# Optimization experiments

Measured on AMD Instinct MI355X. Metric: run time of the kernel, lower is better.

## Reference

```python
import jax, jax.numpy as jnp
import numpy as np

B, C, H, W = 2, 256, 48, 48
HIDDEN, NUM_HEADS = 512, 8
HEAD_DIM = HIDDEN // NUM_HEADS
EPS = 1e-5


def setup_inputs() -> dict:
    key = jax.random.key(0)
    ks = jax.random.split(key, 16)
    inp = {
        'modal1_feat': jax.random.normal(ks[0], (B, C, H, W), jnp.float32),
        'modal2_feat': jax.random.normal(ks[1], (B, C, H, W), jnp.float32),
    }
    s = 0.02  # weight init scale
    names = ['wq1', 'wk1', 'wv1', 'wq2', 'wk2', 'wv2']
    for i, nm in enumerate(names):
        inp[nm] = jax.random.normal(ks[2 + i], (HIDDEN, C), jnp.float32) * s
        inp['b' + nm[1:]] = jnp.zeros((HIDDEN,), jnp.float32)
    inp['wo1'] = jax.random.normal(ks[8], (C, HIDDEN), jnp.float32) * s
    inp['bo1'] = jnp.zeros((C,), jnp.float32)
    inp['wo2'] = jax.random.normal(ks[9], (C, HIDDEN), jnp.float32) * s
    inp['bo2'] = jnp.zeros((C,), jnp.float32)
    inp['ln1_g'] = jnp.ones((C,), jnp.float32)
    inp['ln1_b'] = jnp.zeros((C,), jnp.float32)
    inp['ln2_g'] = jnp.ones((C,), jnp.float32)
    inp['ln2_b'] = jnp.zeros((C,), jnp.float32)
    inp['wf'] = jax.random.normal(ks[10], (C, 2 * C), jnp.float32) * s
    inp['bf'] = jnp.zeros((C,), jnp.float32)
    inp['bn_g'] = jnp.ones((C,), jnp.float32)
    inp['bn_b'] = jnp.zeros((C,), jnp.float32)
    inp['bn_mean'] = jnp.zeros((C,), jnp.float32)
    inp['bn_var'] = jnp.ones((C,), jnp.float32)
    return inp


def _conv1x1(x, w, b):
    return jnp.einsum('bchw,oc->bohw', x, w) + b[None, :, None, None]


def _ln_channels(x, g, b):
    # LayerNorm over channel dim (x: [B,C,H,W]) applied in NHWC layout
    xc = x.transpose(0, 2, 3, 1)
    mu = xc.mean(-1, keepdims=True)
    var = ((xc - mu) ** 2).mean(-1, keepdims=True)
    y = (xc - mu) / jnp.sqrt(var + EPS) * g + b
    return y.transpose(0, 3, 1, 2)


def reference(modal1_feat, modal2_feat, wq1, bq1, wk1, bk1, wv1, bv1,
              wq2, bq2, wk2, bk2, wv2, bv2, wo1, bo1, wo2, bo2,
              ln1_g, ln1_b, ln2_g, ln2_b, wf, bf, bn_g, bn_b, bn_mean, bn_var):
    b_, c1, h1, w1 = modal1_feat.shape
    hw = h1 * w1
    scale = HEAD_DIM ** -0.5

    def as_q(t):  # [B,hidden,H,W] -> [B,h,L,d]
        return t.reshape(b_, NUM_HEADS, HEAD_DIM, hw).transpose(0, 1, 3, 2)

    def as_k(t):  # [B,h,d,L]
        return t.reshape(b_, NUM_HEADS, HEAD_DIM, hw)

    q1 = as_q(_conv1x1(modal1_feat, wq1, bq1))
    k1 = as_k(_conv1x1(modal1_feat, wk1, bk1))
    v1 = as_q(_conv1x1(modal1_feat, wv1, bv1))
    q2 = as_q(_conv1x1(modal2_feat, wq2, bq2))
    k2 = as_k(_conv1x1(modal2_feat, wk2, bk2))
    v2 = as_q(_conv1x1(modal2_feat, wv2, bv2))

    a12 = jax.nn.softmax(jnp.einsum('bhld,bhdm->bhlm', q1, k2) * scale, axis=-1)
    o1 = jnp.einsum('bhlm,bhmd->bhld', a12, v2).transpose(0, 1, 3, 2).reshape(b_, HIDDEN, h1, w1)
    a21 = jax.nn.softmax(jnp.einsum('bhld,bhdm->bhlm', q2, k1) * scale, axis=-1)
    o2 = jnp.einsum('bhlm,bhmd->bhld', a21, v1).transpose(0, 1, 3, 2).reshape(b_, HIDDEN, h1, w1)

    mod1_cross = _conv1x1(o1, wo1, bo1)
    mod2_cross = _conv1x1(o2, wo2, bo2)

    m1 = _ln_channels(modal1_feat + mod1_cross, ln1_g, ln1_b)
    m2 = _ln_channels(modal2_feat + mod2_cross, ln2_g, ln2_b)

    fused = jnp.concatenate([m1, m2], axis=1)
    f = _conv1x1(fused, wf, bf)
    # BatchNorm2d in eval mode (running stats)
    f = (f - bn_mean[None, :, None, None]) / jnp.sqrt(bn_var + EPS)[None, :, None, None]
    f = f * bn_g[None, :, None, None] + bn_b[None, :, None, None]
    return jax.nn.relu(f)
```

## Files before the change

### kernel.cpp

```cpp
#include <hip/hip_runtime.h>
#include <hip/hip_bf16.h>

#define HW_N 2304
#define EPS_F 1e-5f
#define QSCALE 0.18033688011112043f

typedef float f32x4 __attribute__((ext_vector_type(4)));
typedef short short8v __attribute__((ext_vector_type(8)));
typedef __bf16 bf16x8 __attribute__((ext_vector_type(8)));
typedef unsigned short u16;

__device__ __forceinline__ f32x4 mfma_bf16(bf16x8 a, bf16x8 b, f32x4 c) {
    return __builtin_amdgcn_mfma_f32_16x16x32_bf16(a, b, c, 0, 0, 0);
}
__device__ __forceinline__ bf16x8 ld8(const void* p) {
    return __builtin_bit_cast(bf16x8, *(const short8v*)p);
}
__device__ __forceinline__ unsigned short bfbits(float v) {
    return __builtin_bit_cast(unsigned short, __float2bfloat16(v));
}
__device__ __forceinline__ float b2f(u16 u) {
    unsigned x = (unsigned)u << 16;
    return __builtin_bit_cast(float, x);
}
__device__ __forceinline__ unsigned pack2(float lo, float hi) {
    return (unsigned)bfbits(lo) | ((unsigned)bfbits(hi) << 16);
}
__device__ __forceinline__ float max4(f32x4 v) {
    return fmaxf(fmaxf(v.x, v.y), fmaxf(v.z, v.w));
}
__device__ __forceinline__ float sum4(f32x4 v) {
    return (v.x + v.y) + (v.z + v.w);
}

struct WPtrs { const float* s[9]; u16* d[9]; };

__global__ __launch_bounds__(256)
void conv_w_kernel(WPtrs p)
{
    const int j = blockIdx.z;
    const float* s = p.s[j];
    u16* d = p.d[j];
    const int i = (blockIdx.x * 256 + threadIdx.x) * 4;
    const float4 v = *(const float4*)(s + i);
    ushort4 pk;
    pk.x = bfbits(v.x); pk.y = bfbits(v.y); pk.z = bfbits(v.z); pk.w = bfbits(v.w);
    *(ushort4*)(d + i) = pk;
}

__global__ __launch_bounds__(256)
void prep_modal_kernel(const float* __restrict__ m1, const float* __restrict__ m2,
                       u16* __restrict__ t1, u16* __restrict__ t2)
{
    const int l0 = blockIdx.x * 64, c0 = blockIdx.y * 64;
    const int which = blockIdx.z >> 1, b = blockIdx.z & 1;
    const float* src = (which ? m2 : m1) + ((long long)b * 256 + c0) * HW_N + l0;
    u16* dst = (which ? t2 : t1) + ((long long)b * HW_N + l0) * 256 + c0;

    __shared__ float tile[64][65];
    const int t = threadIdx.x;
    const int r = t >> 4, cq = (t & 15) * 4;
#pragma unroll
    for (int i = 0; i < 4; ++i) {
        const int row = r + i * 16;
        const float4 v = *(const float4*)(src + (long long)row * HW_N + cq);
        tile[row][cq + 0] = v.x; tile[row][cq + 1] = v.y;
        tile[row][cq + 2] = v.z; tile[row][cq + 3] = v.w;
    }
    __syncthreads();
#pragma unroll
    for (int i = 0; i < 4; ++i) {
        const int lr = r + i * 16;
        ushort4 pk;
        pk.x = bfbits(tile[cq + 0][lr]);
        pk.y = bfbits(tile[cq + 1][lr]);
        pk.z = bfbits(tile[cq + 2][lr]);
        pk.w = bfbits(tile[cq + 3][lr]);
        *(ushort4*)(dst + (long long)lr * 256 + cq) = pk;
    }
}

struct GArgs {
    const u16* W[6];
    const float* bias[6];
    const u16* X[2];
    const u16* R[2];
    u16* outQ[2]; u16* outK[2]; u16* outV[2];
    float* outT[2];
    float* outC;
    const float *bnm, *bnv, *bng, *bnb;
};

template<int MODE>
__global__ __launch_bounds__(256)
void gemm_mfma(GArgs g)
{
    constexpr int KD = (MODE == 0) ? 256 : 512;
    constexpr int NS = KD / 32;
    const int z = blockIdx.y;
    const int j = blockIdx.z;
    const int mt_b = blockIdx.x / 18;
    const int nt_b = blockIdx.x - mt_b * 18;
    const int m0 = mt_b * 128, n0 = nt_b * 128;

    const u16* Wb = g.W[(MODE == 2) ? 0 : j];
    const u16* Xb0 = (MODE == 0) ? g.X[(j < 3) ? 0 : 1]
                                 : ((MODE == 1) ? g.X[j] : nullptr);

    __shared__ u16 Als[4096];
    __shared__ u16 Bls[4096];

    const int tid = threadIdx.x;
    const int w = tid >> 6, lane = tid & 63;
    const int l16 = lane & 15, lg = lane >> 4;

    const int ar0 = (((tid >> 6) << 4) | (tid & 15));
    const int k8 = (tid >> 4) & 3;

    short8v sa0, sa1, sb0, sb1;

    auto stage = [&](int kb) {
        const int koff = kb + k8 * 8;
        sa0 = *(const short8v*)(Wb + (long long)(m0 + ar0) * KD + koff);
        sa1 = *(const short8v*)(Wb + (long long)(m0 + ar0 + 64) * KD + koff);
        if constexpr (MODE == 0) {
            const u16* p = Xb0 + ((long long)z * HW_N + n0 + ar0) * 256 + koff;
            sb0 = *(const short8v*)p;
            sb1 = *(const short8v*)(p + 64LL * 256);
        } else if constexpr (MODE == 1) {
            const int head = kb >> 6;
            const u16* p = Xb0 + (((long long)z * 8 + head) * HW_N + n0 + ar0) * 64 + (koff & 63);
            sb0 = *(const short8v*)p;
            sb1 = *(const short8v*)(p + 64LL * 64);
        } else {
            const u16* Xb = (kb < 256) ? g.X[0] : g.X[1];
            const u16* p = Xb + ((long long)z * HW_N + n0 + ar0) * 256 + (koff & 255);
            sb0 = *(const short8v*)p;
            sb1 = *(const short8v*)(p + 64LL * 256);
        }
    };

    f32x4 acc[4][4];
#pragma unroll
    for (int a = 0; a < 4; ++a)
#pragma unroll
        for (int b = 0; b < 4; ++b) acc[a][b] = f32x4{0.f, 0.f, 0.f, 0.f};

    stage(0);
    for (int s = 0; s < NS; ++s) {
        __syncthreads();
        *(short8v*)((char*)Als + tid * 16) = sa0;
        *(short8v*)((char*)Als + tid * 16 + 4096) = sa1;
        *(short8v*)((char*)Bls + tid * 16) = sb0;
        *(short8v*)((char*)Bls + tid * 16 + 4096) = sb1;
        __syncthreads();
        if (s + 1 < NS) stage((s + 1) * 32);

        bf16x8 bfr[4];
#pragma unroll
        for (int nt = 0; nt < 4; ++nt)
            bfr[nt] = ld8((char*)Bls + ((w & 1) * 4 + nt) * 1024 + lane * 16);
#pragma unroll
        for (int mt = 0; mt < 4; ++mt) {
            const bf16x8 af = ld8((char*)Als + ((w >> 1) * 4 + mt) * 1024 + lane * 16);
#pragma unroll
            for (int nt = 0; nt < 4; ++nt)
                acc[mt][nt] = mfma_bf16(af, bfr[nt], acc[mt][nt]);
        }
    }

    const int mbase = m0 + (w >> 1) * 64 + 4 * lg;
    const int nbase = n0 + (w & 1) * 64 + l16;

    if constexpr (MODE == 0) {
        const int kind = j % 3, which = j / 3;
        const float* Bp = g.bias[j];
        if (kind < 2) {
            u16* T = (kind == 0) ? g.outQ[which] : g.outK[which];
            const float s = (kind == 0) ? QSCALE : 1.0f;
#pragma unroll
            for (int mt = 0; mt < 4; ++mt) {
                const int m = mbase + mt * 16;
                const float4 bv = *(const float4*)(Bp + m);
#pragma unroll
                for (int nt = 0; nt < 4; ++nt) {
                    const int l = nbase + nt * 16;
                    const f32x4 a = acc[mt][nt];
                    ushort4 pk;
                    pk.x = bfbits((a.x + bv.x) * s);
                    pk.y = bfbits((a.y + bv.y) * s);
                    pk.z = bfbits((a.z + bv.z) * s);
                    pk.w = bfbits((a.w + bv.w) * s);
                    *(ushort4*)(T + ((long long)(z * 8 + (m >> 6)) * HW_N + l) * 64 + (m & 63)) = pk;
                }
            }
        } else {
            u16* V = g.outV[which];
#pragma unroll
            for (int mt = 0; mt < 4; ++mt) {
                const int m = mbase + mt * 16;
                const float4 bv = *(const float4*)(Bp + m);
#pragma unroll
                for (int nt = 0; nt < 4; ++nt) {
                    const int l = nbase + nt * 16;
                    const f32x4 a = acc[mt][nt];
                    V[((long long)z * 512 + m + 0) * HW_N + l] = bfbits(a.x + bv.x);
                    V[((long long)z * 512 + m + 1) * HW_N + l] = bfbits(a.y + bv.y);
                    V[((long long)z * 512 + m + 2) * HW_N + l] = bfbits(a.z + bv.z);
                    V[((long long)z * 512 + m + 3) * HW_N + l] = bfbits(a.w + bv.w);
                }
            }
        }
    } else if constexpr (MODE == 1) {
        const float* Bp = g.bias[j];
        const u16* Rb = g.R[j];
        float* Ob = g.outT[j];
#pragma unroll
        for (int mt = 0; mt < 4; ++mt) {
            const int m = mbase + mt * 16;
            const float4 bv = *(const float4*)(Bp + m);
#pragma unroll
            for (int nt = 0; nt < 4; ++nt) {
                const int l = nbase + nt * 16;
                const long long rowoff = ((long long)z * HW_N + l) * 256 + m;
                const ushort4 rv = *(const ushort4*)(Rb + rowoff);
                const f32x4 a = acc[mt][nt];
                float4 o;
                o.x = a.x + bv.x + b2f(rv.x);
                o.y = a.y + bv.y + b2f(rv.y);
                o.z = a.z + bv.z + b2f(rv.z);
                o.w = a.w + bv.w + b2f(rv.w);
                *(float4*)(Ob + rowoff) = o;
            }
        }
    } else {
        const float* Bp = g.bias[0];
#pragma unroll
        for (int mt = 0; mt < 4; ++mt) {
            const int m = mbase + mt * 16;
            const float4 bv = *(const float4*)(Bp + m);
            const float4 mu = *(const float4*)(g.bnm + m);
            const float4 vr = *(const float4*)(g.bnv + m);
            const float4 ga = *(const float4*)(g.bng + m);
            const float4 be = *(const float4*)(g.bnb + m);
            const float sc0 = ga.x * rsqrtf(vr.x + EPS_F), sh0 = be.x - mu.x * sc0;
            const float sc1 = ga.y * rsqrtf(vr.y + EPS_F), sh1 = be.y - mu.y * sc1;
            const float sc2 = ga.z * rsqrtf(vr.z + EPS_F), sh2 = be.z - mu.z * sc2;
            const float sc3 = ga.w * rsqrtf(vr.w + EPS_F), sh3 = be.w - mu.w * sc3;
#pragma unroll
            for (int nt = 0; nt < 4; ++nt) {
                const int l = nbase + nt * 16;
                const f32x4 a = acc[mt][nt];
                float* O = g.outC + (long long)z * 256 * HW_N + l;
                O[(long long)(m + 0) * HW_N] = fmaxf((a.x + bv.x) * sc0 + sh0, 0.f);
                O[(long long)(m + 1) * HW_N] = fmaxf((a.y + bv.y) * sc1 + sh1, 0.f);
                O[(long long)(m + 2) * HW_N] = fmaxf((a.z + bv.z) * sc2 + sh2, 0.f);
                O[(long long)(m + 3) * HW_N] = fmaxf((a.w + bv.w) * sc3 + sh3, 0.f);
            }
        }
    }
}

__global__ __launch_bounds__(256)
void attn_mfma_kernel(const u16* __restrict__ qt0, const u16* __restrict__ kt0,
                      const u16* __restrict__ v0b,
                      const u16* __restrict__ qt1, const u16* __restrict__ kt1,
                      const u16* __restrict__ v1b,
                      u16* __restrict__ oat0T, u16* __restrict__ oat1T)
{
    const int flat = blockIdx.x;
    const int virt = (flat & 7) * 144 + (flat >> 3);
    const int lt = virt % 36;
    const int h = (virt / 36) & 7;
    const int zz = virt / 288;
    const int b = zz >> 1, dir = zz & 1;

    const u16* QT = dir ? qt1 : qt0;
    const u16* KT = dir ? kt0 : kt1;
    const u16* V  = dir ? v0b : v1b;

    const long long bh = (long long)(b * 8 + h);
    const u16* Qb = QT + bh * HW_N * 64;
    const u16* Kb = KT + bh * HW_N * 64;
    const u16* Vb = V + ((long long)b * 512 + h * 64) * HW_N;

    const int tid = threadIdx.x;
    const int w = tid >> 6, lane = tid & 63;
    const int l16 = lane & 15, lg = lane >> 4;
    const int l0 = lt * 64;

    __shared__ u16 Ks[64 * 64];
    __shared__ u16 Vs[64 * 64];
    __shared__ u16 Ps[4][16 * 72];

    bf16x8 qf0, qf1;
    {
        const u16* qrow = Qb + (long long)(l0 + 16 * w + l16) * 64 + 8 * lg;
        qf0 = ld8(qrow);
        qf1 = ld8(qrow + 32);
    }

    f32x4 acc0 = {0.f, 0.f, 0.f, 0.f}, acc1 = acc0, acc2 = acc0, acc3 = acc0;
    float m_run = -1e30f, s_run = 0.f;

    const int rsub = lane >> 3;
    const int csub = (lane & 7) * 8;
    const int r0 = 16 * w + rsub, r1 = r0 + 8;
    const int swz0 = (csub * 2) ^ ((r0 & 7) << 4);
    const int swz1 = (csub * 2) ^ ((r1 & 7) << 4);
    const int cb0 = (16 * lg) ^ ((l16 & 7) << 4);
    const int cb1 = (16 * lg + 64) ^ ((l16 & 7) << 4);

    short8v ka, kb2, va, vb2;
    {
        const u16* kbase = Kb + (long long)(16 * w) * 64;
        ka  = *(const short8v*)(kbase + (long long)rsub * 64 + csub);
        kb2 = *(const short8v*)(kbase + (long long)(8 + rsub) * 64 + csub);
        const u16* vbase = Vb + (long long)(16 * w + rsub) * HW_N + csub;
        va  = *(const short8v*)(vbase);
        vb2 = *(const short8v*)(vbase + 8LL * HW_N);
    }

    char* prow = (char*)&Ps[w][0] + 144 * l16;

    for (int t = 0; t < 36; ++t) {
        if (t) __syncthreads();
        *(short8v*)((char*)Ks + r0 * 128 + swz0) = ka;
        *(short8v*)((char*)Ks + r1 * 128 + swz1) = kb2;
        *(short8v*)((char*)Vs + r0 * 128 + swz0) = va;
        *(short8v*)((char*)Vs + r1 * 128 + swz1) = vb2;
        __syncthreads();
        if (t + 1 < 36) {
            const int m0 = (t + 1) * 64;
            const u16* kbase = Kb + (long long)(m0 + 16 * w) * 64;
            ka  = *(const short8v*)(kbase + (long long)rsub * 64 + csub);
            kb2 = *(const short8v*)(kbase + (long long)(8 + rsub) * 64 + csub);
            const u16* vbase = Vb + (long long)(16 * w + rsub) * HW_N + m0 + csub;
            va  = *(const short8v*)(vbase);
            vb2 = *(const short8v*)(vbase + 8LL * HW_N);
        }

        const char* kb_ = (const char*)Ks + l16 * 128;
        f32x4 st0 = {0.f,0.f,0.f,0.f}, st1 = st0, st2 = st0, st3 = st0;
        st0 = mfma_bf16(ld8(kb_ + 0 * 2048 + cb0), qf0, st0);
        st0 = mfma_bf16(ld8(kb_ + 0 * 2048 + cb1), qf1, st0);
        st1 = mfma_bf16(ld8(kb_ + 1 * 2048 + cb0), qf0, st1);
        st1 = mfma_bf16(ld8(kb_ + 1 * 2048 + cb1), qf1, st1);
        st2 = mfma_bf16(ld8(kb_ + 2 * 2048 + cb0), qf0, st2);
        st2 = mfma_bf16(ld8(kb_ + 2 * 2048 + cb1), qf1, st2);
        st3 = mfma_bf16(ld8(kb_ + 3 * 2048 + cb0), qf0, st3);
        st3 = mfma_bf16(ld8(kb_ + 3 * 2048 + cb1), qf1, st3);

        float mx = fmaxf(fmaxf(max4(st0), max4(st1)), fmaxf(max4(st2), max4(st3)));
        mx = fmaxf(mx, __shfl_xor(mx, 16, 64));
        mx = fmaxf(mx, __shfl_xor(mx, 32, 64));
        const float m_new = fmaxf(m_run, mx);
        const float alpha = exp2f(m_run - m_new);

        f32x4 p0, p1, p2, p3;
        p0.x = exp2f(st0.x - m_new); p0.y = exp2f(st0.y - m_new);
        p0.z = exp2f(st0.z - m_new); p0.w = exp2f(st0.w - m_new);
        p1.x = exp2f(st1.x - m_new); p1.y = exp2f(st1.y - m_new);
        p1.z = exp2f(st1.z - m_new); p1.w = exp2f(st1.w - m_new);
        p2.x = exp2f(st2.x - m_new); p2.y = exp2f(st2.y - m_new);
        p2.z = exp2f(st2.z - m_new); p2.w = exp2f(st2.w - m_new);
        p3.x = exp2f(st3.x - m_new); p3.y = exp2f(st3.y - m_new);
        p3.z = exp2f(st3.z - m_new); p3.w = exp2f(st3.w - m_new);

        float psum = sum4(p0) + sum4(p1) + sum4(p2) + sum4(p3);
        psum += __shfl_xor(psum, 16, 64);
        psum += __shfl_xor(psum, 32, 64);
        s_run = s_run * alpha + psum;
        m_run = m_new;
        acc0 *= alpha; acc1 *= alpha; acc2 *= alpha; acc3 *= alpha;

        *(unsigned*)(prow + 8 * lg + 0)   = pack2(p0.x, p0.y);
        *(unsigned*)(prow + 8 * lg + 4)   = pack2(p0.z, p0.w);
        *(unsigned*)(prow + 8 * lg + 32)  = pack2(p1.x, p1.y);
        *(unsigned*)(prow + 8 * lg + 36)  = pack2(p1.z, p1.w);
        *(unsigned*)(prow + 8 * lg + 64)  = pack2(p2.x, p2.y);
        *(unsigned*)(prow + 8 * lg + 68)  = pack2(p2.z, p2.w);
        *(unsigned*)(prow + 8 * lg + 96)  = pack2(p3.x, p3.y);
        *(unsigned*)(prow + 8 * lg + 100) = pack2(p3.z, p3.w);

        bf16x8 pf0 = ld8(prow + 16 * lg);
        bf16x8 pf1 = ld8(prow + 64 + 16 * lg);
        const char* vb_ = (const char*)Vs + l16 * 128;
        acc0 = mfma_bf16(ld8(vb_ + 0 * 2048 + cb0), pf0, acc0);
        acc0 = mfma_bf16(ld8(vb_ + 0 * 2048 + cb1), pf1, acc0);
        acc1 = mfma_bf16(ld8(vb_ + 1 * 2048 + cb0), pf0, acc1);
        acc1 = mfma_bf16(ld8(vb_ + 1 * 2048 + cb1), pf1, acc1);
        acc2 = mfma_bf16(ld8(vb_ + 2 * 2048 + cb0), pf0, acc2);
        acc2 = mfma_bf16(ld8(vb_ + 2 * 2048 + cb1), pf1, acc2);
        acc3 = mfma_bf16(ld8(vb_ + 3 * 2048 + cb0), pf0, acc3);
        acc3 = mfma_bf16(ld8(vb_ + 3 * 2048 + cb1), pf1, acc3);
    }

    const float inv = 1.0f / s_run;
    u16* obase = (dir ? oat1T : oat0T) +
                 ((long long)(b * 8 + h) * HW_N + l0 + 16 * w + l16) * 64;
#define OSTORE(T4, A) { \
    ushort4 pk; \
    pk.x = bfbits(A.x * inv); pk.y = bfbits(A.y * inv); \
    pk.z = bfbits(A.z * inv); pk.w = bfbits(A.w * inv); \
    *(ushort4*)(obase + (T4) * 16 + 4 * lg) = pk; }
    OSTORE(0, acc0) OSTORE(1, acc1) OSTORE(2, acc2) OSTORE(3, acc3)
#undef OSTORE
}

__global__ __launch_bounds__(256)
void ln_t_kernel(const float* __restrict__ mpre0T, const float* __restrict__ mpre1T,
                 const float* __restrict__ g1, const float* __restrict__ b1,
                 const float* __restrict__ g2, const float* __restrict__ b2,
                 u16* __restrict__ mln0T, u16* __restrict__ mln1T)
{
    const int l = blockIdx.x * 64 + (threadIdx.x >> 2);
    const int z = blockIdx.y, dir = blockIdx.z;
    const float* src = (dir ? mpre1T : mpre0T) + ((long long)z * HW_N + l) * 256;
    const float* gg = dir ? g2 : g1;
    const float* bb = dir ? b2 : b1;
    u16* dst = (dir ? mln1T : mln0T) + ((long long)z * HW_N + l) * 256;
    const int q = (threadIdx.x & 3) * 64;

    float4 vbuf[16];
    float sum = 0.f, sq = 0.f;
#pragma unroll
    for (int i = 0; i < 16; ++i) {
        const float4 v = *(const float4*)(src + q + i * 4);
        vbuf[i] = v;
        sum += (v.x + v.y) + (v.z + v.w);
        sq += (v.x * v.x + v.y * v.y) + (v.z * v.z + v.w * v.w);
    }
    sum += __shfl_xor(sum, 1, 64); sum += __shfl_xor(sum, 2, 64);
    sq  += __shfl_xor(sq, 1, 64);  sq  += __shfl_xor(sq, 2, 64);
    const float mean = sum * (1.f / 256.f);
    const float var = sq * (1.f / 256.f) - mean * mean;
    const float rstd = rsqrtf(var + EPS_F);
#pragma unroll
    for (int i = 0; i < 16; ++i) {
        const int c = q + i * 4;
        const float4 gv = *(const float4*)(gg + c);
        const float4 bv = *(const float4*)(bb + c);
        ushort4 pk;
        pk.x = bfbits((vbuf[i].x - mean) * rstd * gv.x + bv.x);
        pk.y = bfbits((vbuf[i].y - mean) * rstd * gv.y + bv.y);
        pk.z = bfbits((vbuf[i].z - mean) * rstd * gv.z + bv.z);
        pk.w = bfbits((vbuf[i].w - mean) * rstd * gv.w + bv.w);
        *(ushort4*)(dst + c) = pk;
    }
}

extern "C" void kernel_launch(void* const* d_in, const int* in_sizes, int n_in,
                              void* d_out, int out_size, void* d_ws, size_t ws_size,
                              hipStream_t stream)
{
    (void)in_sizes; (void)n_in; (void)out_size; (void)ws_size;

    const float* modal1 = (const float*)d_in[0];
    const float* modal2 = (const float*)d_in[1];
    const float* wqkv[6]; const float* bqkv[6];
    for (int j = 0; j < 6; ++j) {
        wqkv[j] = (const float*)d_in[2 + 2 * j];
        bqkv[j] = (const float*)d_in[3 + 2 * j];
    }
    const float* wo1 = (const float*)d_in[14];
    const float* bo1 = (const float*)d_in[15];
    const float* wo2 = (const float*)d_in[16];
    const float* bo2 = (const float*)d_in[17];
    const float* ln1_g = (const float*)d_in[18];
    const float* ln1_b = (const float*)d_in[19];
    const float* ln2_g = (const float*)d_in[20];
    const float* ln2_b = (const float*)d_in[21];
    const float* wf = (const float*)d_in[22];
    const float* bf = (const float*)d_in[23];
    const float* bn_g = (const float*)d_in[24];
    const float* bn_b = (const float*)d_in[25];
    const float* bn_mean = (const float*)d_in[26];
    const float* bn_var = (const float*)d_in[27];

    char* ws = (char*)d_ws;
    size_t off = 0;
    auto alloc = [&](size_t bytes) { char* p = ws + off; off += (bytes + 255) & ~(size_t)255; return p; };

    u16* modalT[2]; u16* wbf[9]; u16* qT[2]; u16* kT[2]; u16* vC[2];
    u16* oatT[2]; float* mpreT[2]; u16* mlnT[2];
    for (int i = 0; i < 2; ++i) modalT[i] = (u16*)alloc(2LL * HW_N * 256 * 2);
    for (int i = 0; i < 9; ++i) wbf[i] = (u16*)alloc(131072 * 2);
    for (int i = 0; i < 2; ++i) qT[i] = (u16*)alloc(2LL * 512 * HW_N * 2);
    for (int i = 0; i < 2; ++i) kT[i] = (u16*)alloc(2LL * 512 * HW_N * 2);
    for (int i = 0; i < 2; ++i) vC[i] = (u16*)alloc(2LL * 512 * HW_N * 2);
    for (int i = 0; i < 2; ++i) oatT[i] = (u16*)alloc(2LL * 512 * HW_N * 2);
    for (int i = 0; i < 2; ++i) mpreT[i] = (float*)alloc(2LL * HW_N * 256 * 4);
    for (int i = 0; i < 2; ++i) mlnT[i] = (u16*)alloc(2LL * HW_N * 256 * 2);

    WPtrs wp;
    for (int j = 0; j < 6; ++j) { wp.s[j] = wqkv[j]; wp.d[j] = wbf[j]; }
    wp.s[6] = wo1; wp.d[6] = wbf[6];
    wp.s[7] = wo2; wp.d[7] = wbf[7];
    wp.s[8] = wf;  wp.d[8] = wbf[8];
    conv_w_kernel<<<dim3(128, 1, 9), 256, 0, stream>>>(wp);
    prep_modal_kernel<<<dim3(36, 4, 4), 256, 0, stream>>>(modal1, modal2, modalT[0], modalT[1]);

    GArgs g0 = {};
    for (int j = 0; j < 6; ++j) { g0.W[j] = wbf[j]; g0.bias[j] = bqkv[j]; }
    g0.X[0] = modalT[0]; g0.X[1] = modalT[1];
    for (int i = 0; i < 2; ++i) { g0.outQ[i] = qT[i]; g0.outK[i] = kT[i]; g0.outV[i] = vC[i]; }
    gemm_mfma<0><<<dim3(72, 2, 6), 256, 0, stream>>>(g0);

    attn_mfma_kernel<<<dim3(36 * 8 * 4), 256, 0, stream>>>(
        qT[0], kT[0], vC[0], qT[1], kT[1], vC[1], oatT[0], oatT[1]);

    GArgs g1a = {};
    g1a.W[0] = wbf[6]; g1a.W[1] = wbf[7];
    g1a.bias[0] = bo1; g1a.bias[1] = bo2;
    g1a.X[0] = oatT[0]; g1a.X[1] = oatT[1];
    g1a.R[0] = modalT[0]; g1a.R[1] = modalT[1];
    g1a.outT[0] = mpreT[0]; g1a.outT[1] = mpreT[1];
    gemm_mfma<1><<<dim3(36, 2, 2), 256, 0, stream>>>(g1a);

    ln_t_kernel<<<dim3(36, 2, 2), 256, 0, stream>>>(
        mpreT[0], mpreT[1], ln1_g, ln1_b, ln2_g, ln2_b, mlnT[0], mlnT[1]);

    GArgs g2a = {};
    g2a.W[0] = wbf[8]; g2a.bias[0] = bf;
    g2a.X[0] = mlnT[0]; g2a.X[1] = mlnT[1];
    g2a.outC = (float*)d_out;
    g2a.bnm = bn_mean; g2a.bnv = bn_var; g2a.bng = bn_g; g2a.bnb = bn_b;
    gemm_mfma<2><<<dim3(36, 2, 1), 256, 0, stream>>>(g2a);
}
```

Measured before the change: 195.0 us.

## Double-buffer K/V tiles in attention, lazy rescale, MFMA row sums, swizzled P

The flash-attention loop now uses double-buffered shared K/V tiles with a two-stage register prefetch, leaving one barrier per iteration instead of two. The online softmax skips the rescale unless the new max exceeds the running max by more than a threshold. Row sums are computed by an extra MFMA against a ones vector instead of shuffle reductions. The P scratch gets an XOR swizzle to cut bank conflicts, and s_setprio is placed around the MFMA blocks. The cost is twice the shared memory for K/V, two extra MFMAs per tile, and softmax sums accumulated from the bf16-rounded probabilities.

```diff
diff --git a/kernel.cpp b/kernel.cpp
--- a/kernel.cpp
+++ b/kernel.cpp
@@ -28,9 +28,6 @@
 }
 __device__ __forceinline__ float max4(f32x4 v) {
     return fmaxf(fmaxf(v.x, v.y), fmaxf(v.z, v.w));
-}
-__device__ __forceinline__ float sum4(f32x4 v) {
-    return (v.x + v.y) + (v.z + v.w);
 }
 
 struct WPtrs { const float* s[9]; u16* d[9]; };
@@ -289,9 +286,9 @@
     const int l16 = lane & 15, lg = lane >> 4;
     const int l0 = lt * 64;
 
-    __shared__ u16 Ks[64 * 64];
-    __shared__ u16 Vs[64 * 64];
-    __shared__ u16 Ps[4][16 * 72];
+    __shared__ u16 Ks[2][64 * 64];
+    __shared__ u16 Vs[2][64 * 64];
+    __shared__ u16 Ps[4][16 * 64];
 
     bf16x8 qf0, qf1;
     {
@@ -299,9 +296,17 @@
         qf0 = ld8(qrow);
         qf1 = ld8(qrow + 32);
     }
+    bf16x8 onesv;
+    {
+        short8v o;
+#pragma unroll
+        for (int i = 0; i < 8; ++i) o[i] = (short)0x3F80;
+        onesv = __builtin_bit_cast(bf16x8, o);
+    }
 
     f32x4 acc0 = {0.f, 0.f, 0.f, 0.f}, acc1 = acc0, acc2 = acc0, acc3 = acc0;
-    float m_run = -1e30f, s_run = 0.f;
+    f32x4 accs = acc0;
+    float m_run = -1e30f;
 
     const int rsub = lane >> 3;
     const int csub = (lane & 7) * 8;
@@ -312,36 +317,41 @@
     const int cb1 = (16 * lg + 64) ^ ((l16 & 7) << 4);
 
     short8v ka, kb2, va, vb2;
-    {
-        const u16* kbase = Kb + (long long)(16 * w) * 64;
+    auto stage = [&](int t) {
+        const int m0 = t * 64;
+        const u16* kbase = Kb + (long long)(m0 + 16 * w) * 64;
         ka  = *(const short8v*)(kbase + (long long)rsub * 64 + csub);
         kb2 = *(const short8v*)(kbase + (long long)(8 + rsub) * 64 + csub);
-        const u16* vbase = Vb + (long long)(16 * w + rsub) * HW_N + csub;
+        const u16* vbase = Vb + (long long)(16 * w + rsub) * HW_N + m0 + csub;
         va  = *(const short8v*)(vbase);
         vb2 = *(const short8v*)(vbase + 8LL * HW_N);
-    }
-
-    char* prow = (char*)&Ps[w][0] + 144 * l16;
+    };
+    auto commit = [&](int buf) {
+        *(short8v*)((char*)Ks[buf] + r0 * 128 + swz0) = ka;
+        *(short8v*)((char*)Ks[buf] + r1 * 128 + swz1) = kb2;
+        *(short8v*)((char*)Vs[buf] + r0 * 128 + swz0) = va;
+        *(short8v*)((char*)Vs[buf] + r1 * 128 + swz1) = vb2;
+    };
+
+    char* Pw = (char*)&Ps[w][0];
+    const int pxor = l16 & 7;
+    const int pw_hi = lg >> 1;
+    const int pw_lo = 8 * (lg & 1);
+    const int prow = l16 * 128;
+    const int pr0 = prow + ((lg ^ pxor) << 4);
+    const int pr1 = prow + (((4 + lg) ^ pxor) << 4);
+
+    stage(0); commit(0); stage(1);
+    __syncthreads();
 
     for (int t = 0; t < 36; ++t) {
-        if (t) __syncthreads();
-        *(short8v*)((char*)Ks + r0 * 128 + swz0) = ka;
-        *(short8v*)((char*)Ks + r1 * 128 + swz1) = kb2;
-        *(short8v*)((char*)Vs + r0 * 128 + swz0) = va;
-        *(short8v*)((char*)Vs + r1 * 128 + swz1) = vb2;
-        __syncthreads();
-        if (t + 1 < 36) {
-            const int m0 = (t + 1) * 64;
-            const u16* kbase = Kb + (long long)(m0 + 16 * w) * 64;
-            ka  = *(const short8v*)(kbase + (long long)rsub * 64 + csub);
-            kb2 = *(const short8v*)(kbase + (long long)(8 + rsub) * 64 + csub);
-            const u16* vbase = Vb + (long long)(16 * w + rsub) * HW_N + m0 + csub;
-            va  = *(const short8v*)(vbase);
-            vb2 = *(const short8v*)(vbase + 8LL * HW_N);
-        }
-
-        const char* kb_ = (const char*)Ks + l16 * 128;
+        const int cur = t & 1;
+        if (t + 1 < 36) commit(cur ^ 1);
+        if (t + 2 < 36) stage(t + 2);
+
+        const char* kb_ = (const char*)Ks[cur] + l16 * 128;
         f32x4 st0 = {0.f,0.f,0.f,0.f}, st1 = st0, st2 = st0, st3 = st0;
+        __builtin_amdgcn_s_setprio(1);
         st0 = mfma_bf16(ld8(kb_ + 0 * 2048 + cb0), qf0, st0);
         st0 = mfma_bf16(ld8(kb_ + 0 * 2048 + cb1), qf1, st0);
         st1 = mfma_bf16(ld8(kb_ + 1 * 2048 + cb0), qf0, st1);
@@ -350,42 +360,45 @@
         st2 = mfma_bf16(ld8(kb_ + 2 * 2048 + cb1), qf1, st2);
         st3 = mfma_bf16(ld8(kb_ + 3 * 2048 + cb0), qf0, st3);
         st3 = mfma_bf16(ld8(kb_ + 3 * 2048 + cb1), qf1, st3);
+        __builtin_amdgcn_s_setprio(0);
 
         float mx = fmaxf(fmaxf(max4(st0), max4(st1)), fmaxf(max4(st2), max4(st3)));
         mx = fmaxf(mx, __shfl_xor(mx, 16, 64));
         mx = fmaxf(mx, __shfl_xor(mx, 32, 64));
-        const float m_new = fmaxf(m_run, mx);
-        const float alpha = exp2f(m_run - m_new);
+        if (!__all(mx <= m_run + 8.f)) {
+            const float m_new = fmaxf(m_run, mx);
+            const float alpha = exp2f(m_run - m_new);
+            acc0 *= alpha; acc1 *= alpha; acc2 *= alpha; acc3 *= alpha;
+            accs *= alpha;
+            m_run = m_new;
+        }
 
         f32x4 p0, p1, p2, p3;
-        p0.x = exp2f(st0.x - m_new); p0.y = exp2f(st0.y - m_new);
-        p0.z = exp2f(st0.z - m_new); p0.w = exp2f(st0.w - m_new);
-        p1.x = exp2f(st1.x - m_new); p1.y = exp2f(st1.y - m_new);
-        p1.z = exp2f(st1.z - m_new); p1.w = exp2f(st1.w - m_new);
-        p2.x = exp2f(st2.x - m_new); p2.y = exp2f(st2.y - m_new);
-        p2.z = exp2f(st2.z - m_new); p2.w = exp2f(st2.w - m_new);
-        p3.x = exp2f(st3.x - m_new); p3.y = exp2f(st3.y - m_new);
-        p3.z = exp2f(st3.z - m_new); p3.w = exp2f(st3.w - m_new);
-
-        float psum = sum4(p0) + sum4(p1) + sum4(p2) + sum4(p3);
-        psum += __shfl_xor(psum, 16, 64);
-        psum += __shfl_xor(psum, 32, 64);
-        s_run = s_run * alpha + psum;
-        m_run = m_new;
-        acc0 *= alpha; acc1 *= alpha; acc2 *= alpha; acc3 *= alpha;
-
-        *(unsigned*)(prow + 8 * lg + 0)   = pack2(p0.x, p0.y);
-        *(unsigned*)(prow + 8 * lg + 4)   = pack2(p0.z, p0.w);
-        *(unsigned*)(prow + 8 * lg + 32)  = pack2(p1.x, p1.y);
-        *(unsigned*)(prow + 8 * lg + 36)  = pack2(p1.z, p1.w);
-        *(unsigned*)(prow + 8 * lg + 64)  = pack2(p2.x, p2.y);
-        *(unsigned*)(prow + 8 * lg + 68)  = pack2(p2.z, p2.w);
-        *(unsigned*)(prow + 8 * lg + 96)  = pack2(p3.x, p3.y);
-        *(unsigned*)(prow + 8 * lg + 100) = pack2(p3.z, p3.w);
-
-        bf16x8 pf0 = ld8(prow + 16 * lg);
-        bf16x8 pf1 = ld8(prow + 64 + 16 * lg);
-        const char* vb_ = (const char*)Vs + l16 * 128;
+        p0.x = exp2f(st0.x - m_run); p0.y = exp2f(st0.y - m_run);
+        p0.z = exp2f(st0.z - m_run); p0.w = exp2f(st0.w - m_run);
+        p1.x = exp2f(st1.x - m_run); p1.y = exp2f(st1.y - m_run);
+        p1.z = exp2f(st1.z - m_run); p1.w = exp2f(st1.w - m_run);
+        p2.x = exp2f(st2.x - m_run); p2.y = exp2f(st2.y - m_run);
+        p2.z = exp2f(st2.z - m_run); p2.w = exp2f(st2.w - m_run);
+        p3.x = exp2f(st3.x - m_run); p3.y = exp2f(st3.y - m_run);
+        p3.z = exp2f(st3.z - m_run); p3.w = exp2f(st3.w - m_run);
+
+        {
+            uint2 u;
+            u.x = pack2(p0.x, p0.y); u.y = pack2(p0.z, p0.w);
+            *(uint2*)(Pw + prow + (((0 + pw_hi) ^ pxor) << 4) + pw_lo) = u;
+            u.x = pack2(p1.x, p1.y); u.y = pack2(p1.z, p1.w);
+            *(uint2*)(Pw + prow + (((2 + pw_hi) ^ pxor) << 4) + pw_lo) = u;
+            u.x = pack2(p2.x, p2.y); u.y = pack2(p2.z, p2.w);
+            *(uint2*)(Pw + prow + (((4 + pw_hi) ^ pxor) << 4) + pw_lo) = u;
+            u.x = pack2(p3.x, p3.y); u.y = pack2(p3.z, p3.w);
+            *(uint2*)(Pw + prow + (((6 + pw_hi) ^ pxor) << 4) + pw_lo) = u;
+        }
+
+        bf16x8 pf0 = ld8(Pw + pr0);
+        bf16x8 pf1 = ld8(Pw + pr1);
+        const char* vb_ = (const char*)Vs[cur] + l16 * 128;
+        __builtin_amdgcn_s_setprio(1);
         acc0 = mfma_bf16(ld8(vb_ + 0 * 2048 + cb0), pf0, acc0);
         acc0 = mfma_bf16(ld8(vb_ + 0 * 2048 + cb1), pf1, acc0);
         acc1 = mfma_bf16(ld8(vb_ + 1 * 2048 + cb0), pf0, acc1);
@@ -394,9 +407,14 @@
         acc2 = mfma_bf16(ld8(vb_ + 2 * 2048 + cb1), pf1, acc2);
         acc3 = mfma_bf16(ld8(vb_ + 3 * 2048 + cb0), pf0, acc3);
         acc3 = mfma_bf16(ld8(vb_ + 3 * 2048 + cb1), pf1, acc3);
-    }
-
-    const float inv = 1.0f / s_run;
+        accs = mfma_bf16(onesv, pf0, accs);
+        accs = mfma_bf16(onesv, pf1, accs);
+        __builtin_amdgcn_s_setprio(0);
+
+        __syncthreads();
+    }
+
+    const float inv = 1.0f / accs.x;
     u16* obase = (dir ? oat1T : oat0T) +
                  ((long long)(b * 8 + h) * HW_N + l0 + 16 * w + l16) * 64;
 #define OSTORE(T4, A) { \
```

New measurement: 173.8 us. -10.9%, faster.
